# Optimization experiments

Measured on AMD Instinct MI355X. Metric: run time of the kernel, lower is better.

Reference implementation:

```python
import jax, jax.numpy as jnp
import numpy as np

B, T, D = 2, 2048, 2048
H, HD = 16, 128
I = 5632
CAP = 0.5
EPS = 1e-6
NEG = -1e9


def _rmsnorm(x, w):
    v = x.astype(jnp.float32)
    v = v * jax.lax.rsqrt(jnp.mean(v * v, axis=-1, keepdims=True) + EPS)
    return v.astype(x.dtype) * w


def _rotate_half(x):
    x1, x2 = jnp.split(x, 2, axis=-1)
    return jnp.concatenate([-x2, x1], axis=-1)


def setup_inputs() -> dict:
    key = jax.random.key(0)
    ks = jax.random.split(key, 20)
    s = 0.02
    inp = {
        'hidden_states': jax.random.normal(ks[0], (B, T, D), jnp.float32),
        'original': jax.random.normal(ks[1], (B, T, D), jnp.float32),
        'posterior': jax.random.normal(ks[2], (B, T, D), jnp.float32),
        'prior': jax.random.normal(ks[3], (B, T, D), jnp.float32),
        'cos': jax.random.normal(ks[4], (B, T, HD), jnp.float32),
        'sin': jax.random.normal(ks[5], (B, T, HD), jnp.float32),
        'position_ids': jax.random.randint(ks[6], (B, T), 0, T),
        'q_w': jax.random.normal(ks[7], (D, H * HD), jnp.float32) * s,
        'q_b': jnp.zeros((H * HD,), jnp.float32),
        'k_w': jax.random.normal(ks[8], (D, H * HD), jnp.float32) * s,
        'k_b': jnp.zeros((H * HD,), jnp.float32),
        'v_w': jax.random.normal(ks[9], (D, H * HD), jnp.float32) * s,
        'v_b': jnp.zeros((H * HD,), jnp.float32),
        'o_w': jax.random.normal(ks[10], (H * HD, D), jnp.float32) * s,
        'ln1_w': jnp.ones((D,), jnp.float32),
        'ln2_w': jnp.ones((D,), jnp.float32),
        'gate_w': jax.random.normal(ks[11], (D, I), jnp.float32) * s,
        'up_w': jax.random.normal(ks[12], (D, I), jnp.float32) * s,
        'down_w': jax.random.normal(ks[13], (I, D), jnp.float32) * s,
        'beta_ce': jnp.array(-0.5, jnp.float32),
        'beta_cu': jnp.array(-0.8, jnp.float32),
        'ce_off': jnp.array(1.0, jnp.float32),
    }
    return inp


def reference(hidden_states, original, posterior, prior, cos, sin, position_ids,
              q_w, q_b, k_w, k_b, v_w, v_b, o_w, ln1_w, ln2_w,
              gate_w, up_w, down_w, beta_ce, beta_cu, ce_off):
    Bt, Tt, Dt = hidden_states.shape
    K = int(CAP * Tt)  # tokens selected per batch row
    # --- router: surprise scores ---
    cu = jnp.linalg.norm(original - posterior, axis=-1)  # [B,T]
    ce = jnp.linalg.norm(posterior - prior, axis=-1)     # [B,T]
    scores = beta_cu * cu + beta_ce * (ce + ce_off)      # [B,T]
    # --- capacity top-k per batch row, keep temporal order ---
    _, topi = jax.lax.top_k(scores, K)                   # [B,K]
    token_idx2 = jnp.sort(topi, axis=-1)                 # [B,K]
    sel_scores = jnp.take_along_axis(scores, token_idx2, axis=1)  # [B,K]
    b_idx = jnp.repeat(jnp.arange(Bt), K)                # [S]
    t_idx = token_idx2.reshape(-1)                       # [S]
    S = Bt * K
    sel_h = hidden_states[b_idx, t_idx]                  # [S,D]
    cos_g = cos[b_idx, t_idx][None, None]                # [1,1,S,HD]
    sin_g = sin[b_idx, t_idx][None, None]
    # --- Qwen2 decoder block on the single gathered sequence [1,S,D] ---
    x = sel_h[None]
    h = _rmsnorm(x, ln1_w)
    q = (h @ q_w + q_b).reshape(1, S, H, HD).transpose(0, 2, 1, 3)  # [1,H,S,HD]
    k = (h @ k_w + k_b).reshape(1, S, H, HD).transpose(0, 2, 1, 3)
    v = (h @ v_w + v_b).reshape(1, S, H, HD).transpose(0, 2, 1, 3)
    q = q * cos_g + _rotate_half(q) * sin_g
    k = k * cos_g + _rotate_half(k) * sin_g
    att = jnp.einsum('bhqd,bhkd->bhqk', q, k) / np.sqrt(HD)
    causal = jnp.tril(jnp.ones((S, S), bool))
    att = jnp.where(causal, att, NEG)
    att = jax.nn.softmax(att.astype(jnp.float32), axis=-1).astype(x.dtype)
    o = jnp.einsum('bhqk,bhkd->bhqd', att, v)
    o = o.transpose(0, 2, 1, 3).reshape(1, S, H * HD) @ o_w
    x = x + o
    h = _rmsnorm(x, ln2_w)
    mlp = (jax.nn.silu(h @ gate_w) * (h @ up_w)) @ down_w
    x = x + mlp
    processed = x[0]                                     # [S,D]
    # --- gated update + scatter back ---
    gate = jax.nn.sigmoid(sel_scores.reshape(-1))[:, None]
    updated = sel_h + (processed - sel_h) * gate
    output = hidden_states.at[b_idx, t_idx].set(updated)
    return output
```

## Files before the change

### kernel.cpp

```cpp
#include <hip/hip_runtime.h>


typedef unsigned short u16;
typedef unsigned int u32;
typedef short bf16x8 __attribute__((ext_vector_type(8)));
typedef float f32x4 __attribute__((ext_vector_type(4)));

#define T_LEN 2048
#define D_DIM 2048
#define B_DIM 2
#define H_NUM 16
#define HD_DIM 128
#define I_DIM 5632
#define K_CAP 1024
#define S_TOT 2048
#define QKV_N 6144
#define GU_N 11264

__device__ __forceinline__ u16 f2bf(float f) {
  union { float f; u32 u; } a; a.f = f;
  u32 r = a.u + 0x7fffu + ((a.u >> 16) & 1u);
  return (u16)(r >> 16);
}
__device__ __forceinline__ float bf2f(u16 x) {
  return __uint_as_float((u32)x << 16);
}

__device__ __forceinline__ void gld_lds16(const void* g, void* l) {
  void* gg = const_cast<void*>(g);
  __builtin_amdgcn_global_load_lds(
      (__attribute__((address_space(1))) u32*)gg,
      (__attribute__((address_space(3))) u32*)l, 16, 0, 0);
}

__global__ __launch_bounds__(256)
void router_kernel(const float* __restrict__ orig, const float* __restrict__ post,
                   const float* __restrict__ prior, const float* __restrict__ bce,
                   const float* __restrict__ bcu, const float* __restrict__ coff,
                   float* __restrict__ scores) {
  const int row = blockIdx.x;
  const size_t base = (size_t)row * D_DIM;
  float s1 = 0.f, s2 = 0.f;
  for (int d = threadIdx.x * 4; d < D_DIM; d += 1024) {
    float4 o = *(const float4*)(orig + base + d);
    float4 p = *(const float4*)(post + base + d);
    float4 r = *(const float4*)(prior + base + d);
    float a;
    a = o.x - p.x; s1 += a * a;  a = o.y - p.y; s1 += a * a;
    a = o.z - p.z; s1 += a * a;  a = o.w - p.w; s1 += a * a;
    a = p.x - r.x; s2 += a * a;  a = p.y - r.y; s2 += a * a;
    a = p.z - r.z; s2 += a * a;  a = p.w - r.w; s2 += a * a;
  }
#pragma unroll
  for (int k = 32; k; k >>= 1) { s1 += __shfl_down(s1, k); s2 += __shfl_down(s2, k); }
  __shared__ float r1[4], r2[4];
  const int wv = threadIdx.x >> 6;
  if ((threadIdx.x & 63) == 0) { r1[wv] = s1; r2[wv] = s2; }
  __syncthreads();
  if (threadIdx.x == 0) {
    float cu = sqrtf(r1[0] + r1[1] + r1[2] + r1[3]);
    float ce = sqrtf(r2[0] + r2[1] + r2[2] + r2[3]);
    scores[row] = bcu[0] * cu + bce[0] * (ce + coff[0]);
  }
}

__global__ __launch_bounds__(256)
void rank_kernel(const float* __restrict__ scores, int* __restrict__ rnk) {
  const int b = blockIdx.y;
  const int t = blockIdx.x * 256 + threadIdx.x;
  __shared__ float s[T_LEN];
  for (int u = threadIdx.x; u < T_LEN; u += 256) s[u] = scores[b * T_LEN + u];
  __syncthreads();
  const float st = s[t];
  int r = 0;
  for (int u = 0; u < T_LEN; ++u) {
    float su = s[u];
    r += ((su > st) || (su == st && u < t)) ? 1 : 0;
  }
  rnk[b * T_LEN + t] = r;
}

__global__ __launch_bounds__(256)
void compact_kernel(const float* __restrict__ scores, const int* __restrict__ rnk,
                    int* __restrict__ tidx, float* __restrict__ gate) {
  const int b = blockIdx.x;
  const int base = b * T_LEN;
  __shared__ int csum[256];
  int f[8]; int loc = 0;
  const int t0 = threadIdx.x * 8;
#pragma unroll
  for (int i = 0; i < 8; ++i) { f[i] = (rnk[base + t0 + i] < K_CAP) ? 1 : 0; loc += f[i]; }
  csum[threadIdx.x] = loc;
  __syncthreads();
  if (threadIdx.x == 0) {
    int run = 0;
    for (int i = 0; i < 256; ++i) { int tmp = csum[i]; csum[i] = run; run += tmp; }
  }
  __syncthreads();
  int pos = csum[threadIdx.x];
#pragma unroll
  for (int i = 0; i < 8; ++i) {
    if (f[i]) {
      float sc = scores[base + t0 + i];
      tidx[b * K_CAP + pos] = t0 + i;
      gate[b * K_CAP + pos] = 1.f / (1.f + __expf(-sc));
      ++pos;
    }
  }
}

__global__ __launch_bounds__(256)
void transpose_bf16_kernel(const float* __restrict__ W, u16* __restrict__ Wt,
                           int K, int N) {
  __shared__ float tile[32][33];
  const int bn = blockIdx.x * 32, bk = blockIdx.y * 32;
  const int tx = threadIdx.x & 31, ty = threadIdx.x >> 5;
#pragma unroll
  for (int i = 0; i < 32; i += 8)
    tile[ty + i][tx] = W[(size_t)(bk + ty + i) * N + bn + tx];
  __syncthreads();
#pragma unroll
  for (int i = 0; i < 32; i += 8)
    Wt[(size_t)(bn + ty + i) * K + bk + tx] = f2bf(tile[tx][ty + i]);
}

__global__ __launch_bounds__(256)
void vtrans_kernel(const u16* __restrict__ qkv, u16* __restrict__ VT) {
  __shared__ u16 tile[32][34];
  const int s0 = blockIdx.x * 32;
  const int c0 = blockIdx.y * 32;
  const int tx = threadIdx.x & 31, ty = threadIdx.x >> 5;
#pragma unroll
  for (int i = 0; i < 32; i += 8)
    tile[ty + i][tx] = qkv[(size_t)(s0 + ty + i) * QKV_N + 4096 + c0 + tx];
  __syncthreads();
#pragma unroll
  for (int i = 0; i < 32; i += 8)
    VT[(size_t)(c0 + ty + i) * S_TOT + s0 + tx] = tile[tx][ty + i];
}

__global__ __launch_bounds__(256)
void rmsnorm_kernel(const float* __restrict__ X, const int* __restrict__ tidx,
                    const float* __restrict__ w, float* __restrict__ xcopy,
                    u16* __restrict__ Y) {
  const int s = blockIdx.x;
  const float* row;
  if (tidx) {
    const int b = s >> 10;
    const int t = tidx[s];
    row = X + ((size_t)b * T_LEN + t) * D_DIM;
  } else {
    row = X + (size_t)s * D_DIM;
  }
  const int d0 = threadIdx.x * 4;
  float4 v0 = *(const float4*)(row + d0);
  float4 v1 = *(const float4*)(row + d0 + 1024);
  float ss = v0.x*v0.x + v0.y*v0.y + v0.z*v0.z + v0.w*v0.w
           + v1.x*v1.x + v1.y*v1.y + v1.z*v1.z + v1.w*v1.w;
#pragma unroll
  for (int k = 32; k; k >>= 1) ss += __shfl_down(ss, k);
  __shared__ float red[4];
  if ((threadIdx.x & 63) == 0) red[threadIdx.x >> 6] = ss;
  __syncthreads();
  const float tot = red[0] + red[1] + red[2] + red[3];
  const float rms = rsqrtf(tot * (1.0f / D_DIM) + 1e-6f);
  if (xcopy) {
    *(float4*)(xcopy + (size_t)s * D_DIM + d0) = v0;
    *(float4*)(xcopy + (size_t)s * D_DIM + d0 + 1024) = v1;
  }
  const float4 w0 = *(const float4*)(w + d0);
  const float4 w1 = *(const float4*)(w + d0 + 1024);
  u16* yp = Y + (size_t)s * D_DIM;
  u32 a0 = (u32)f2bf(v0.x * rms * w0.x) | ((u32)f2bf(v0.y * rms * w0.y) << 16);
  u32 a1 = (u32)f2bf(v0.z * rms * w0.z) | ((u32)f2bf(v0.w * rms * w0.w) << 16);
  *(uint2*)(yp + d0) = make_uint2(a0, a1);
  u32 b0 = (u32)f2bf(v1.x * rms * w1.x) | ((u32)f2bf(v1.y * rms * w1.y) << 16);
  u32 b1 = (u32)f2bf(v1.z * rms * w1.z) | ((u32)f2bf(v1.w * rms * w1.w) << 16);
  *(uint2*)(yp + d0 + 1024) = make_uint2(b0, b1);
}

__global__ __launch_bounds__(256)
void gemm_bf16_kernel(const u16* __restrict__ A, const u16* __restrict__ Bt,
                      float* __restrict__ C, u16* __restrict__ Cbf,
                      const float* __restrict__ bias,
                      const float* __restrict__ resid, int N, int K) {
  __shared__ u16 As[128 * 32];
  __shared__ u16 Bs[128 * 32];
  const int tid = threadIdx.x;
  const int w = tid >> 6, l = tid & 63;
  const int row0 = blockIdx.y * 128, col0 = blockIdx.x * 128;
  const int wr = (w >> 1) * 64, wc = (w & 1) * 64;
  const int am = l & 15, ak = (l >> 4) * 8;
  const int srow = l >> 2, scol = (l & 3) * 8;

  f32x4 acc[4][4] = {};

  const u16* Abase = A + (size_t)(row0 + srow) * K + scol;
  const u16* Bbase = Bt + (size_t)(col0 + srow) * K + scol;
  const int R0 = (w * 2) * 16, R1 = (w * 2 + 1) * 16;

  for (int k0 = 0; k0 < K; k0 += 32) {
    gld_lds16(Abase + (size_t)R0 * K + k0, &As[R0 * 32]);
    gld_lds16(Abase + (size_t)R1 * K + k0, &As[R1 * 32]);
    gld_lds16(Bbase + (size_t)R0 * K + k0, &Bs[R0 * 32]);
    gld_lds16(Bbase + (size_t)R1 * K + k0, &Bs[R1 * 32]);
    __syncthreads();
    bf16x8 af[4], bfr[4];
#pragma unroll
    for (int i = 0; i < 4; ++i) af[i] = *(const bf16x8*)&As[(wr + i * 16 + am) * 32 + ak];
#pragma unroll
    for (int j = 0; j < 4; ++j) bfr[j] = *(const bf16x8*)&Bs[(wc + j * 16 + am) * 32 + ak];
#pragma unroll
    for (int i = 0; i < 4; ++i)
#pragma unroll
      for (int j = 0; j < 4; ++j)
        acc[i][j] = __builtin_amdgcn_mfma_f32_16x16x32_bf16(af[i], bfr[j], acc[i][j], 0, 0, 0);
    __syncthreads();
  }

  const int rb = wr + (l >> 4) * 4;
  const int cb = wc + (l & 15);
#pragma unroll
  for (int i = 0; i < 4; ++i) {
#pragma unroll
    for (int j = 0; j < 4; ++j) {
      const int colg = col0 + cb + j * 16;
      const float bv = bias ? bias[colg] : 0.0f;
#pragma unroll
      for (int r = 0; r < 4; ++r) {
        const int rowg = row0 + rb + i * 16 + r;
        const size_t idx = (size_t)rowg * N + colg;
        float v = acc[i][j][r] + bv;
        if (resid) v += resid[idx];
        if (Cbf) Cbf[idx] = f2bf(v);
        else C[idx] = v;
      }
    }
  }
}

__global__ __launch_bounds__(256)
void rope_kernel(u16* __restrict__ qkv, const float* __restrict__ cosb,
                 const float* __restrict__ sinb, const int* __restrict__ tidx) {
  const int idx = blockIdx.x * 256 + threadIdx.x;
  const int d = idx & 63;
  const int h = (idx >> 6) & 15;
  const int s = idx >> 10;
  const int b = s >> 10;
  const int t = tidx[s];
  const size_t base = (size_t)s * QKV_N + h * 128 + d;
  const size_t cb = ((size_t)b * T_LEN + t) * HD_DIM + d;
  const float c1 = cosb[cb], sn1 = sinb[cb];
  const float c2 = cosb[cb + 64], sn2 = sinb[cb + 64];
  float x1v, x2v;
  x1v = bf2f(qkv[base]); x2v = bf2f(qkv[base + 64]);
  qkv[base] = f2bf(x1v * c1 - x2v * sn1);
  qkv[base + 64] = f2bf(x2v * c2 + x1v * sn2);
  x1v = bf2f(qkv[base + 2048]); x2v = bf2f(qkv[base + 2048 + 64]);
  qkv[base + 2048] = f2bf(x1v * c1 - x2v * sn1);
  qkv[base + 2048 + 64] = f2bf(x2v * c2 + x1v * sn2);
}

__global__ __launch_bounds__(512, 4)
void attn_mfma_kernel(const u16* __restrict__ QKV, const u16* __restrict__ VT,
                      u16* __restrict__ Og) {
  const int h  = blockIdx.y;
  const int bx = blockIdx.x;
  const int qt = (h < 8) ? (31 - bx) : bx;
  const int q0 = qt * 64;
  const int tid = threadIdx.x;
  const int l  = tid & 63;
  const int w  = tid >> 6;
  const int g  = w >> 2;
  const int wq = w & 3;
  const int lm = l & 15, lk = l >> 4;

  __shared__ __align__(16) unsigned char smem[65536];
  u16* Ks = (u16*)(smem + g * 16384);
  u16* Vt = (u16*)(smem + 32768 + g * 16384);
  u16* Ps = (u16*)(smem + g * 16384);

  const u16* Qg  = QKV + h * 128;
  const u16* Kg  = QKV + 2048 + h * 128;
  const u16* Vgt = VT + (size_t)h * 128 * S_TOT;

  bf16x8 qf[4];
  {
    const u16* qrow = Qg + (size_t)(q0 + wq * 16 + lm) * QKV_N;
#pragma unroll
    for (int ks = 0; ks < 4; ++ks) qf[ks] = *(const bf16x8*)&qrow[ks * 32 + lk * 8];
  }

  int ksrc[4], vsrc[4];
#pragma unroll
  for (int p = 0; p < 4; ++p) {
    const int ci = (wq * 4 + p) * 64 + l;
    const int kr = ci >> 4, kc = ci & 15;
    ksrc[p] = kr * QKV_N + ((kc ^ (kr & 7)) * 8);
    const int vr = ci >> 3, vc = ci & 7;
    vsrc[p] = vr * S_TOT + ((vc ^ (vr & 7)) * 8);
  }

  f32x4 oacc[8];
#pragma unroll
  for (int n = 0; n < 8; ++n) oacc[n] = (f32x4){0.f, 0.f, 0.f, 0.f};
  float m_run[4] = {-1e30f, -1e30f, -1e30f, -1e30f};
  float l_run[4] = {0.f, 0.f, 0.f, 0.f};

  const int ntiles = (g == 0) ? (qt / 2 + 1) : ((qt + 1) / 2);
  const int nmax = qt / 2 + 1;
  const float scale = 0.08838834764831845f;

  for (int it = 0; it < nmax; ++it) {
    const int kt = g + 2 * it;
    const int kv0 = kt * 64;
    const bool active = (it < ntiles);
    __syncthreads();
    if (active) {
#pragma unroll
      for (int p = 0; p < 4; ++p) {
        gld_lds16(Kg + (size_t)kv0 * QKV_N + ksrc[p], &Ks[(wq * 4 + p) * 512]);
        gld_lds16(Vgt + kv0 + vsrc[p],               &Vt[(wq * 4 + p) * 512]);
      }
    }
    __syncthreads();

    f32x4 sacc[4];
    if (active) {
#pragma unroll
      for (int j = 0; j < 4; ++j) sacc[j] = (f32x4){0.f, 0.f, 0.f, 0.f};
#pragma unroll
      for (int j = 0; j < 4; ++j) {
        const int row = j * 16 + lm;
#pragma unroll
        for (int ks = 0; ks < 4; ++ks) {
          const int c = ks * 4 + lk;
          const bf16x8 kf = *(const bf16x8*)&(
              (const unsigned char*)Ks)[row * 256 + ((c ^ (row & 7)) << 4)];
          sacc[j] = __builtin_amdgcn_mfma_f32_16x16x32_bf16(qf[ks], kf, sacc[j], 0, 0, 0);
        }
      }
    }
    __syncthreads();

    if (active) {
      float mx[4] = {-1e30f, -1e30f, -1e30f, -1e30f};
#pragma unroll
      for (int j = 0; j < 4; ++j) {
        const int colg = kv0 + j * 16 + lm;
#pragma unroll
        for (int r = 0; r < 4; ++r) {
          const int rowg = q0 + wq * 16 + lk * 4 + r;
          float s = sacc[j][r] * scale;
          s = (colg > rowg) ? -1e30f : s;
          sacc[j][r] = s;
          mx[r] = fmaxf(mx[r], s);
        }
      }
#pragma unroll
      for (int r = 0; r < 4; ++r)
#pragma unroll
        for (int dlt = 1; dlt < 16; dlt <<= 1)
          mx[r] = fmaxf(mx[r], __shfl_xor(mx[r], dlt));
      float alpha[4];
#pragma unroll
      for (int r = 0; r < 4; ++r) {
        const float mnew = fmaxf(m_run[r], mx[r]);
        const float al = __expf(m_run[r] - mnew);
        float sum = 0.f;
#pragma unroll
        for (int j = 0; j < 4; ++j) {
          const float pe = __expf(sacc[j][r] - mnew);
          sacc[j][r] = pe;
          sum += pe;
        }
#pragma unroll
        for (int dlt = 1; dlt < 16; dlt <<= 1) sum += __shfl_xor(sum, dlt);
        l_run[r] = l_run[r] * al + sum;
        m_run[r] = mnew;
        alpha[r] = al;
      }
#pragma unroll
      for (int n = 0; n < 8; ++n)
#pragma unroll
        for (int r = 0; r < 4; ++r) oacc[n][r] *= alpha[r];

#pragma unroll
      for (int j = 0; j < 4; ++j)
#pragma unroll
        for (int r = 0; r < 4; ++r) {
          const int row = wq * 16 + lk * 4 + r;
          *(u16*)&((unsigned char*)Ps)[row * 128 +
              (((j * 16 + lm) * 2) ^ ((row & 7) << 4))] = f2bf(sacc[j][r]);
        }

#pragma unroll
      for (int ks2 = 0; ks2 < 2; ++ks2) {
        const int prow = wq * 16 + lm;
        const bf16x8 pf = *(const bf16x8*)&(
            (const unsigned char*)Ps)[prow * 128 +
                ((ks2 * 64 + lk * 16) ^ ((prow & 7) << 4))];
#pragma unroll
        for (int n = 0; n < 8; ++n) {
          const int vrow = n * 16 + lm;
          const int vc = ks2 * 4 + lk;
          const bf16x8 vf = *(const bf16x8*)&(
              (const unsigned char*)Vt)[vrow * 128 + ((vc ^ (vrow & 7)) << 4)];
          oacc[n] = __builtin_amdgcn_mfma_f32_16x16x32_bf16(pf, vf, oacc[n], 0, 0, 0);
        }
      }
    }
  }

  __syncthreads();
  float* Obuf = (float*)smem;
  float* Mbuf = (float*)(smem + 33792);
  float* Lbuf = (float*)(smem + 34048);
  if (g == 1) {
#pragma unroll
    for (int r = 0; r < 4; ++r) {
      const int row = wq * 16 + lk * 4 + r;
      if (lm == 0) { Mbuf[row] = m_run[r]; Lbuf[row] = l_run[r]; }
#pragma unroll
      for (int n = 0; n < 8; ++n) Obuf[row * 132 + n * 16 + lm] = oacc[n][r];
    }
  }
  __syncthreads();
  if (g == 0) {
    float a0[4], a1[4], linv[4];
#pragma unroll
    for (int r = 0; r < 4; ++r) {
      const int row = wq * 16 + lk * 4 + r;
      const float m1 = Mbuf[row], l1 = Lbuf[row];
      const float M = fmaxf(m_run[r], m1);
      a0[r] = __expf(m_run[r] - M);
      a1[r] = __expf(m1 - M);
      linv[r] = 1.f / (a0[r] * l_run[r] + a1[r] * l1);
    }
#pragma unroll
    for (int n = 0; n < 8; ++n)
#pragma unroll
      for (int r = 0; r < 4; ++r) {
        const int row = wq * 16 + lk * 4 + r;
        const float o = (oacc[n][r] * a0[r] +
                         Obuf[row * 132 + n * 16 + lm] * a1[r]) * linv[r];
        Og[(size_t)(q0 + row) * 2048 + h * 128 + n * 16 + lm] = f2bf(o);
      }
  }
}

__global__ __launch_bounds__(256)
void silu_mul_kernel(const u16* __restrict__ gu, u16* __restrict__ out) {
  const size_t i = (size_t)blockIdx.x * 256 + threadIdx.x;
  const int s = (int)(i / 1408);
  const int c = (int)(i - (size_t)s * 1408);
  const uint2 g4 = *(const uint2*)&gu[(size_t)s * GU_N + c * 4];
  const uint2 u4 = *(const uint2*)&gu[(size_t)s * GU_N + I_DIM + c * 4];
  float g[4], u[4];
  g[0] = __uint_as_float(g4.x << 16); g[1] = __uint_as_float(g4.x & 0xffff0000u);
  g[2] = __uint_as_float(g4.y << 16); g[3] = __uint_as_float(g4.y & 0xffff0000u);
  u[0] = __uint_as_float(u4.x << 16); u[1] = __uint_as_float(u4.x & 0xffff0000u);
  u[2] = __uint_as_float(u4.y << 16); u[3] = __uint_as_float(u4.y & 0xffff0000u);
  u16 r[4];
#pragma unroll
  for (int j = 0; j < 4; ++j) r[j] = f2bf(g[j] * u[j] / (1.f + __expf(-g[j])));
  u32 a0 = (u32)r[0] | ((u32)r[1] << 16);
  u32 a1 = (u32)r[2] | ((u32)r[3] << 16);
  *(uint2*)&out[(size_t)s * I_DIM + c * 4] = make_uint2(a0, a1);
}

__global__ __launch_bounds__(256)
void scatter_kernel(const float* __restrict__ hs, const float* __restrict__ x2,
                    const int* __restrict__ tidx, const float* __restrict__ gate,
                    float* __restrict__ out) {
  const int s = blockIdx.x;
  const int b = s >> 10;
  const int t = tidx[s];
  const float gg = gate[s];
  const size_t src = (size_t)s * D_DIM;
  const size_t dst = ((size_t)b * T_LEN + t) * D_DIM;
  for (int d = threadIdx.x * 4; d < D_DIM; d += 1024) {
    float4 hv = *(const float4*)(hs + dst + d);
    float4 pv = *(const float4*)(x2 + src + d);
    float4 r;
    r.x = hv.x + (pv.x - hv.x) * gg;
    r.y = hv.y + (pv.y - hv.y) * gg;
    r.z = hv.z + (pv.z - hv.z) * gg;
    r.w = hv.w + (pv.w - hv.w) * gg;
    *(float4*)(out + dst + d) = r;
  }
}

extern "C" void kernel_launch(void* const* d_in, const int* in_sizes, int n_in,
                              void* d_out, int out_size, void* d_ws, size_t ws_size,
                              hipStream_t stream) {
  (void)in_sizes; (void)n_in; (void)out_size; (void)ws_size;
  const float* hs    = (const float*)d_in[0];
  const float* orig  = (const float*)d_in[1];
  const float* post  = (const float*)d_in[2];
  const float* prior = (const float*)d_in[3];
  const float* cosb  = (const float*)d_in[4];
  const float* sinb  = (const float*)d_in[5];
  const float* q_w = (const float*)d_in[7];
  const float* q_b = (const float*)d_in[8];
  const float* k_w = (const float*)d_in[9];
  const float* k_b = (const float*)d_in[10];
  const float* v_w = (const float*)d_in[11];
  const float* v_b = (const float*)d_in[12];
  const float* o_w = (const float*)d_in[13];
  const float* ln1 = (const float*)d_in[14];
  const float* ln2 = (const float*)d_in[15];
  const float* gate_w = (const float*)d_in[16];
  const float* up_w   = (const float*)d_in[17];
  const float* down_w = (const float*)d_in[18];
  const float* beta_ce = (const float*)d_in[19];
  const float* beta_cu = (const float*)d_in[20];
  const float* ce_off  = (const float*)d_in[21];
  float* out = (float*)d_out;

  char* wsp = (char*)d_ws;
  size_t off = 0;
  auto alloc = [&](size_t n) -> char* {
    char* r = wsp + off; off += (n + 255) & ~(size_t)255; return r;
  };
  const size_t SD4 = (size_t)S_TOT * D_DIM * 4;

  float* scores  = (float*)alloc((size_t)B_DIM * T_LEN * 4);
  int*   rnk     = (int*)  alloc((size_t)B_DIM * T_LEN * 4);
  int*   tidx    = (int*)  alloc((size_t)S_TOT * 4);
  float* gatebuf = (float*)alloc((size_t)S_TOT * 4);
  float* qkvbias = (float*)alloc((size_t)QKV_N * 4);
  u16* qkvwt = (u16*)alloc((size_t)QKV_N * 2048 * 2);
  u16* owt   = (u16*)alloc((size_t)2048 * 2048 * 2);
  u16* guwt  = (u16*)alloc((size_t)GU_N * 2048 * 2);
  u16* dwt   = (u16*)alloc((size_t)2048 * I_DIM * 2);
  char* rA = alloc(SD4);
  float* selh = (float*)rA;
  u16*   h2   = (u16*)rA;
  char* rB = alloc((size_t)S_TOT * I_DIM * 2);
  u16* h1     = (u16*)rB;
  u16* o_attn = (u16*)rB;
  u16* mlp_in = (u16*)rB;
  char* rC = alloc((size_t)S_TOT * GU_N * 2);
  u16* qkv_bf = (u16*)rC;
  u16* gu_bf  = (u16*)rC;
  float* x2   = (float*)rC;
  float* x1 = (float*)alloc(SD4);
  u16* vT = (u16*)x1;

  hipMemcpyAsync(out, hs, (size_t)B_DIM * T_LEN * D_DIM * 4,
                 hipMemcpyDeviceToDevice, stream);
  hipMemcpyAsync(qkvbias, q_b, 2048 * 4, hipMemcpyDeviceToDevice, stream);
  hipMemcpyAsync(qkvbias + 2048, k_b, 2048 * 4, hipMemcpyDeviceToDevice, stream);
  hipMemcpyAsync(qkvbias + 4096, v_b, 2048 * 4, hipMemcpyDeviceToDevice, stream);

  router_kernel<<<dim3(B_DIM * T_LEN), 256, 0, stream>>>(orig, post, prior,
                                                         beta_ce, beta_cu, ce_off, scores);
  rank_kernel<<<dim3(8, B_DIM), 256, 0, stream>>>(scores, rnk);
  compact_kernel<<<dim3(B_DIM), 256, 0, stream>>>(scores, rnk, tidx, gatebuf);

  transpose_bf16_kernel<<<dim3(64, 64), 256, 0, stream>>>(q_w, qkvwt, 2048, 2048);
  transpose_bf16_kernel<<<dim3(64, 64), 256, 0, stream>>>(k_w, qkvwt + (size_t)2048 * 2048, 2048, 2048);
  transpose_bf16_kernel<<<dim3(64, 64), 256, 0, stream>>>(v_w, qkvwt + (size_t)4096 * 2048, 2048, 2048);
  transpose_bf16_kernel<<<dim3(64, 64), 256, 0, stream>>>(o_w, owt, 2048, 2048);
  transpose_bf16_kernel<<<dim3(176, 64), 256, 0, stream>>>(gate_w, guwt, 2048, I_DIM);
  transpose_bf16_kernel<<<dim3(176, 64), 256, 0, stream>>>(up_w, guwt + (size_t)I_DIM * 2048, 2048, I_DIM);
  transpose_bf16_kernel<<<dim3(64, 176), 256, 0, stream>>>(down_w, dwt, I_DIM, 2048);

  rmsnorm_kernel<<<dim3(S_TOT), 256, 0, stream>>>(hs, tidx, ln1, selh, h1);

  gemm_bf16_kernel<<<dim3(48, 16), 256, 0, stream>>>(h1, qkvwt, nullptr, qkv_bf,
                                                     qkvbias, nullptr, QKV_N, 2048);
  rope_kernel<<<dim3((S_TOT * H_NUM * 64) / 256), 256, 0, stream>>>(qkv_bf, cosb, sinb, tidx);

  vtrans_kernel<<<dim3(64, 64), 256, 0, stream>>>(qkv_bf, vT);

  attn_mfma_kernel<<<dim3(32, H_NUM), 512, 0, stream>>>(qkv_bf, vT, o_attn);

  gemm_bf16_kernel<<<dim3(16, 16), 256, 0, stream>>>(o_attn, owt, x1, nullptr,
                                                     nullptr, selh, 2048, 2048);

  rmsnorm_kernel<<<dim3(S_TOT), 256, 0, stream>>>(x1, nullptr, ln2, nullptr, h2);

  gemm_bf16_kernel<<<dim3(88, 16), 256, 0, stream>>>(h2, guwt, nullptr, gu_bf,
                                                     nullptr, nullptr, GU_N, 2048);

  silu_mul_kernel<<<dim3((S_TOT * (I_DIM / 4)) / 256), 256, 0, stream>>>(gu_bf, mlp_in);

  gemm_bf16_kernel<<<dim3(16, 16), 256, 0, stream>>>(mlp_in, dwt, x2, nullptr,
                                                     nullptr, x1, 2048, I_DIM);

  scatter_kernel<<<dim3(S_TOT), 256, 0, stream>>>(hs, x2, tidx, gatebuf, out);
}
```

Measured before the change: 996.6 us.

## Split-K the output and down projections and fuse the reduction into the scatter

Adds a split-K bf16 MFMA GEMM that writes two fp32 partial planes, so the o-proj and down-proj GEMMs launch 512 blocks instead of 256. The two partials plus the residual are summed by a new add3 kernel for the o-proj. For the down-proj, the sum is folded into a new finish kernel that also does the gated scatter, and this replaces the old scatter kernel. The aim is to fill more of the GPU's compute units on these N=2048 GEMMs, paying for it with extra fp32 partial-sum traffic. The o-proj second plane is written past x1 and relies on x1p being allocated right after it in the workspace.

```diff
diff --git a/kernel.cpp b/kernel.cpp
--- a/kernel.cpp
+++ b/kernel.cpp
@@ -236,6 +236,96 @@
         else C[idx] = v;
       }
     }
+  }
+}
+
+__global__ __launch_bounds__(256)
+void gemm_bf16_splitk_kernel(const u16* __restrict__ A, const u16* __restrict__ Bt,
+                             float* __restrict__ P, int N, int K, int kLen) {
+  __shared__ u16 As[128 * 32];
+  __shared__ u16 Bs[128 * 32];
+  const int tid = threadIdx.x;
+  const int w = tid >> 6, l = tid & 63;
+  const int row0 = blockIdx.y * 128, col0 = blockIdx.x * 128;
+  const int kbeg = blockIdx.z * kLen, kend = kbeg + kLen;
+  float* Pz = P + (size_t)blockIdx.z * S_TOT * N;
+  const int wr = (w >> 1) * 64, wc = (w & 1) * 64;
+  const int am = l & 15, ak = (l >> 4) * 8;
+  const int srow = l >> 2, scol = (l & 3) * 8;
+
+  f32x4 acc[4][4] = {};
+
+  const u16* Abase = A + (size_t)(row0 + srow) * K + scol;
+  const u16* Bbase = Bt + (size_t)(col0 + srow) * K + scol;
+  const int R0 = (w * 2) * 16, R1 = (w * 2 + 1) * 16;
+
+  for (int k0 = kbeg; k0 < kend; k0 += 32) {
+    gld_lds16(Abase + (size_t)R0 * K + k0, &As[R0 * 32]);
+    gld_lds16(Abase + (size_t)R1 * K + k0, &As[R1 * 32]);
+    gld_lds16(Bbase + (size_t)R0 * K + k0, &Bs[R0 * 32]);
+    gld_lds16(Bbase + (size_t)R1 * K + k0, &Bs[R1 * 32]);
+    __syncthreads();
+    bf16x8 af[4], bfr[4];
+#pragma unroll
+    for (int i = 0; i < 4; ++i) af[i] = *(const bf16x8*)&As[(wr + i * 16 + am) * 32 + ak];
+#pragma unroll
+    for (int j = 0; j < 4; ++j) bfr[j] = *(const bf16x8*)&Bs[(wc + j * 16 + am) * 32 + ak];
+#pragma unroll
+    for (int i = 0; i < 4; ++i)
+#pragma unroll
+      for (int j = 0; j < 4; ++j)
+        acc[i][j] = __builtin_amdgcn_mfma_f32_16x16x32_bf16(af[i], bfr[j], acc[i][j], 0, 0, 0);
+    __syncthreads();
+  }
+
+  const int rb = wr + (l >> 4) * 4;
+  const int cb = wc + (l & 15);
+#pragma unroll
+  for (int i = 0; i < 4; ++i)
+#pragma unroll
+    for (int j = 0; j < 4; ++j) {
+      const int colg = col0 + cb + j * 16;
+#pragma unroll
+      for (int r = 0; r < 4; ++r) {
+        const int rowg = row0 + rb + i * 16 + r;
+        Pz[(size_t)rowg * N + colg] = acc[i][j][r];
+      }
+    }
+}
+
+__global__ __launch_bounds__(256)
+void add3_kernel(float* __restrict__ acc, const float* __restrict__ p1,
+                 const float* __restrict__ resid) {
+  const size_t i = ((size_t)blockIdx.x * 256 + threadIdx.x) * 4;
+  float4 a = *(const float4*)(acc + i);
+  float4 b = *(const float4*)(p1 + i);
+  float4 c = *(const float4*)(resid + i);
+  a.x += b.x + c.x; a.y += b.y + c.y; a.z += b.z + c.z; a.w += b.w + c.w;
+  *(float4*)(acc + i) = a;
+}
+
+__global__ __launch_bounds__(256)
+void down_finish_kernel(const float* __restrict__ P, const float* __restrict__ x1,
+                        const int* __restrict__ tidx, const float* __restrict__ gate,
+                        const float* __restrict__ hs, float* __restrict__ out) {
+  const int s = blockIdx.x;
+  const int b = s >> 10;
+  const int t = tidx[s];
+  const float gg = gate[s];
+  const size_t src = (size_t)s * D_DIM;
+  const size_t dst = ((size_t)b * T_LEN + t) * D_DIM;
+  const size_t plane = (size_t)S_TOT * D_DIM;
+  for (int d = threadIdx.x * 4; d < D_DIM; d += 1024) {
+    float4 p0 = *(const float4*)(P + src + d);
+    float4 p1 = *(const float4*)(P + plane + src + d);
+    float4 xr = *(const float4*)(x1 + src + d);
+    float4 hv = *(const float4*)(hs + dst + d);
+    float4 r;
+    r.x = hv.x + (p0.x + p1.x + xr.x - hv.x) * gg;
+    r.y = hv.y + (p0.y + p1.y + xr.y - hv.y) * gg;
+    r.z = hv.z + (p0.z + p1.z + xr.z - hv.z) * gg;
+    r.w = hv.w + (p0.w + p1.w + xr.w - hv.w) * gg;
+    *(float4*)(out + dst + d) = r;
   }
 }
 
@@ -467,28 +557,6 @@
   u32 a0 = (u32)r[0] | ((u32)r[1] << 16);
   u32 a1 = (u32)r[2] | ((u32)r[3] << 16);
   *(uint2*)&out[(size_t)s * I_DIM + c * 4] = make_uint2(a0, a1);
-}
-
-__global__ __launch_bounds__(256)
-void scatter_kernel(const float* __restrict__ hs, const float* __restrict__ x2,
-                    const int* __restrict__ tidx, const float* __restrict__ gate,
-                    float* __restrict__ out) {
-  const int s = blockIdx.x;
-  const int b = s >> 10;
-  const int t = tidx[s];
-  const float gg = gate[s];
-  const size_t src = (size_t)s * D_DIM;
-  const size_t dst = ((size_t)b * T_LEN + t) * D_DIM;
-  for (int d = threadIdx.x * 4; d < D_DIM; d += 1024) {
-    float4 hv = *(const float4*)(hs + dst + d);
-    float4 pv = *(const float4*)(x2 + src + d);
-    float4 r;
-    r.x = hv.x + (pv.x - hv.x) * gg;
-    r.y = hv.y + (pv.y - hv.y) * gg;
-    r.z = hv.z + (pv.z - hv.z) * gg;
-    r.w = hv.w + (pv.w - hv.w) * gg;
-    *(float4*)(out + dst + d) = r;
-  }
 }
 
 extern "C" void kernel_launch(void* const* d_in, const int* in_sizes, int n_in,
@@ -544,8 +612,10 @@
   char* rC = alloc((size_t)S_TOT * GU_N * 2);
   u16* qkv_bf = (u16*)rC;
   u16* gu_bf  = (u16*)rC;
-  float* x2   = (float*)rC;
-  float* x1 = (float*)alloc(SD4);
+  float* dpart = (float*)rC;
+  float* x1  = (float*)alloc(SD4);
+  float* x1p = (float*)alloc(SD4);
+  (void)x1p;
   u16* vT = (u16*)x1;
 
   hipMemcpyAsync(out, hs, (size_t)B_DIM * T_LEN * D_DIM * 4,
@@ -577,8 +647,10 @@
 
   attn_mfma_kernel<<<dim3(32, H_NUM), 512, 0, stream>>>(qkv_bf, vT, o_attn);
 
-  gemm_bf16_kernel<<<dim3(16, 16), 256, 0, stream>>>(o_attn, owt, x1, nullptr,
-                                                     nullptr, selh, 2048, 2048);
+  gemm_bf16_splitk_kernel<<<dim3(16, 16, 2), 256, 0, stream>>>(o_attn, owt, x1,
+                                                               2048, 2048, 1024);
+  add3_kernel<<<dim3((S_TOT * D_DIM) / 1024), 256, 0, stream>>>(
+      x1, x1 + (size_t)S_TOT * D_DIM, selh);
 
   rmsnorm_kernel<<<dim3(S_TOT), 256, 0, stream>>>(x1, nullptr, ln2, nullptr, h2);
 
@@ -587,8 +659,9 @@
 
   silu_mul_kernel<<<dim3((S_TOT * (I_DIM / 4)) / 256), 256, 0, stream>>>(gu_bf, mlp_in);
 
-  gemm_bf16_kernel<<<dim3(16, 16), 256, 0, stream>>>(mlp_in, dwt, x2, nullptr,
-                                                     nullptr, x1, 2048, I_DIM);
-
-  scatter_kernel<<<dim3(S_TOT), 256, 0, stream>>>(hs, x2, tidx, gatebuf, out);
-}
+  gemm_bf16_splitk_kernel<<<dim3(16, 16, 2), 256, 0, stream>>>(mlp_in, dwt, dpart,
+                                                               2048, 5632, 2816);
+
+  down_finish_kernel<<<dim3(S_TOT), 256, 0, stream>>>(dpart, x1, tidx, gatebuf,
+                                                      hs, out);
+}
```

After: 923.1 us. 1.08x faster.
